# Performance work log

Hardware: AMD Instinct MI355X
Metric: run time of the kernel (lower is better)

The kernel has to match this reference:

```python
import jax, jax.numpy as jnp
import numpy as np

DIM = 512
FEAT = 64
BATCH = 2048

def setup_inputs() -> dict:
    key = jax.random.key(0)
    kx, kw, kb = jax.random.split(key, 3)
    x = jax.random.normal(kx, (BATCH, DIM, FEAT), dtype=jnp.float32)
    # torch Linear weight is [out, in]; emulate Kaiming-uniform-ish init scale
    bound = 1.0 / np.sqrt(FEAT)
    W = jax.random.uniform(kw, (DIM, FEAT, FEAT), dtype=jnp.float32, minval=-bound, maxval=bound)
    b = jax.random.uniform(kb, (DIM, FEAT), dtype=jnp.float32, minval=-bound, maxval=bound)
    return {"x": x, "W": W, "b": b}

def reference(x, W, b):
    # per-slice Linear: out[:, d, :] = x[:, d, :] @ W[d].T + b[d]
    # fused as one batched contraction over the feature (input) axis 'f'
    return jnp.einsum('bdf,dgf->bdg', x, W) + b[None, :, :]
```

## Files before the change

kernel.cpp:

```cpp
#include <hip/hip_runtime.h>
#include <hip/hip_bf16.h>

#define DIM  512
#define FEAT 64
#define BATCH 2048

#define DPB    64
#define NTILES 16

using bf16x8 = __attribute__((ext_vector_type(8))) short;
using f32x4  = __attribute__((ext_vector_type(4))) float;

typedef __attribute__((address_space(3))) float lds_f;
typedef __attribute__((address_space(1))) const float glb_f;

__device__ inline short f2bf(float f) {
    unsigned int u = __float_as_uint(f);
    u += 0x7fffu + ((u >> 16) & 1u);
    return (short)(u >> 16);
}

__device__ inline bf16x8 cvt8(float4 a, float4 b) {
    bf16x8 r;
    r[0] = f2bf(a.x); r[1] = f2bf(a.y); r[2] = f2bf(a.z); r[3] = f2bf(a.w);
    r[4] = f2bf(b.x); r[5] = f2bf(b.y); r[6] = f2bf(b.z); r[7] = f2bf(b.w);
    return r;
}

__global__ __launch_bounds__(256)
void w_prep(const float* __restrict__ W, short* __restrict__ ws) {
    const int d = blockIdx.x;
    const int t = threadIdx.x;
    const int l = t & 63, g0 = t >> 6;
#pragma unroll
    for (int h = 0; h < 2; ++h) {
        const int g8 = g0 + h * 4;
        const int mt = g8 & 3, ks = g8 >> 2;
        const float* src = W + ((size_t)d * FEAT + mt * 16 + (l & 15)) * FEAT
                             + ks * 32 + (l >> 4) * 8;
        *(bf16x8*)(ws + ((size_t)(d * 8 + g8) * 64 + l) * 8)
            = cvt8(*(const float4*)src, *(const float4*)(src + 4));
    }
}

template<bool PRE>
__global__ __launch_bounds__(256, 2)
void split_linear_main(const float* __restrict__ x,
                       const float* __restrict__ W,
                       const short* __restrict__ Wb,
                       const float* __restrict__ bias,
                       float* __restrict__ out)
{
    __shared__ float slot[2][16][256];

    const int id = blockIdx.x;
    const int dc = id & 7;
    const int rc = id >> 3;
    const int d0 = dc * DPB;
    const int b0 = rc * 16;

    const int tid  = threadIdx.x;
    const int wave = tid >> 6;
    const int lane = tid & 63;
    const int lr   = lane & 15;
    const int lk   = lane >> 4;

    auto stage = [&](int s, int t) {
#pragma unroll
        for (int i = 0; i < 4; ++i) {
            const int r = wave * 4 + i;
            const float* gp = x + ((size_t)(b0 + r) * DIM + d0 + t * 4) * FEAT
                                + (lane >> 4) * 64 + (((lane & 15) ^ (r & 7)) << 2);
            __builtin_amdgcn_global_load_lds((glb_f*)gp, (lds_f*)&slot[s][r][0], 16, 0, 0);
        }
    };

    const short* wbp = Wb + ((size_t)(d0 + wave)) * 4096 + lane * 8;
    const float* bsp = bias + (size_t)d0 * FEAT + lane * 4;

    auto LOADW = [&](bf16x8 (&wf)[8], f32x4& bv, int t) {
        if (PRE) {
            const short* wq = wbp + (size_t)t * 4 * 4096;
#pragma unroll
            for (int g = 0; g < 8; ++g)
                wf[g] = *(const bf16x8*)(wq + g * 512);
        } else {
            const float* wq = W + (size_t)(d0 + t * 4 + wave) * FEAT * FEAT;
#pragma unroll
            for (int g = 0; g < 8; ++g) {
                const int mt = g & 3, ks = g >> 2;
                const float* p = wq + (size_t)(mt * 16 + lr) * FEAT + ks * 32 + lk * 8;
                wf[g] = cvt8(*(const float4*)p, *(const float4*)(p + 4));
            }
        }
        bv = *(const f32x4*)(bsp + t * 256);
    };

    auto BODY = [&](bf16x8 (&wfc)[8], bf16x8 (&wfn)[8], f32x4& bvc, f32x4& bvn, int t) {
        const int s = t & 1;
        if (t == 0 || t == NTILES - 1)
            asm volatile("s_waitcnt vmcnt(4)" ::: "memory");
        else
            asm volatile("s_waitcnt vmcnt(8)" ::: "memory");
        __builtin_amdgcn_s_barrier();
        __builtin_amdgcn_sched_barrier(0);

        if (t + 1 < NTILES) LOADW(wfn, bvn, t + 1);

        const float* sl = &slot[s][0][0];
        const int rbase = lr * 256 + wave * 64;
        float4 p0a = *(const float4*)&sl[rbase + (((lk * 2 + 0) ^ (lr & 7)) << 2)];
        float4 p0b = *(const float4*)&sl[rbase + (((lk * 2 + 1) ^ (lr & 7)) << 2)];
        float4 p1a = *(const float4*)&sl[rbase + (((8 + lk * 2 + 0) ^ (lr & 7)) << 2)];
        float4 p1b = *(const float4*)&sl[rbase + (((8 + lk * 2 + 1) ^ (lr & 7)) << 2)];

        bf16x8 af0 = cvt8(p0a, p0b);
        bf16x8 af1 = cvt8(p1a, p1b);

        f32x4 acc[4] = {{0.f,0.f,0.f,0.f},{0.f,0.f,0.f,0.f},
                        {0.f,0.f,0.f,0.f},{0.f,0.f,0.f,0.f}};
#pragma unroll
        for (int mt = 0; mt < 4; ++mt)
            acc[mt] = __builtin_amdgcn_mfma_f32_16x16x32_bf16(wfc[mt],     af0, acc[mt], 0, 0, 0);
#pragma unroll
        for (int mt = 0; mt < 4; ++mt)
            acc[mt] = __builtin_amdgcn_mfma_f32_16x16x32_bf16(wfc[4 + mt], af1, acc[mt], 0, 0, 0);

        asm volatile("s_waitcnt lgkmcnt(0)" ::: "memory");
        __builtin_amdgcn_s_barrier();
        __builtin_amdgcn_sched_barrier(0);

        float* slw = &slot[s][0][0];
#pragma unroll
        for (int mt = 0; mt < 4; ++mt) {
            const int pc = (mt * 4 + lk) ^ (lr & 7);
            *(f32x4*)&slw[lr * 256 + wave * 64 + pc * 4] = acc[mt];
        }
        asm volatile("s_waitcnt lgkmcnt(0)" ::: "memory");
        __builtin_amdgcn_s_barrier();
        __builtin_amdgcn_sched_barrier(0);

#pragma unroll
        for (int j = 0; j < 4; ++j) {
            const int r = wave * 4 + j;
            f32x4 v = *(const f32x4*)&slw[r * 256 + (lane >> 4) * 64
                                          + (((lane & 15) ^ (r & 7)) << 2)];
            v += bvc;
            __builtin_nontemporal_store(v,
                (f32x4*)(out + ((size_t)(b0 + r) * DIM + d0 + t * 4) * FEAT + lane * 4));
        }
        __builtin_amdgcn_sched_barrier(0);
        if (t + 2 < NTILES) stage(s, t + 2);
        __builtin_amdgcn_sched_barrier(0);
    };

    bf16x8 wfA[8], wfB[8];
    f32x4 bvA, bvB;

    stage(0, 0);
    __builtin_amdgcn_sched_barrier(0);
    LOADW(wfA, bvA, 0);
    __builtin_amdgcn_sched_barrier(0);
    stage(1, 1);
    __builtin_amdgcn_sched_barrier(0);

#pragma unroll
    for (int t = 0; t < NTILES; t += 2) {
        BODY(wfA, wfB, bvA, bvB, t);
        BODY(wfB, wfA, bvB, bvA, t + 1);
    }
}

extern "C" void kernel_launch(void* const* d_in, const int* in_sizes, int n_in,
                              void* d_out, int out_size, void* d_ws, size_t ws_size,
                              hipStream_t stream) {
    const float* x    = (const float*)d_in[0];
    const float* W    = (const float*)d_in[1];
    const float* bias = (const float*)d_in[2];
    float* out        = (float*)d_out;

    const size_t WSNEED = (size_t)DIM * 8 * 64 * 8 * sizeof(short);
    dim3 block(256, 1, 1);
    dim3 grid((BATCH / 16) * (DIM / DPB), 1, 1);

    if (ws_size >= WSNEED) {
        short* ws = (short*)d_ws;
        w_prep<<<dim3(DIM), block, 0, stream>>>(W, ws);
        split_linear_main<true><<<grid, block, 0, stream>>>(x, nullptr, ws, bias, out);
    } else {
        split_linear_main<false><<<grid, block, 0, stream>>>(x, W, nullptr, bias, out);
    }
}
```

Before: 120.6 us.

## Give each wave private LDS slices and batch rows, dropping block barriers

Work is split so each block handles 16 d-slices and 64 batch rows, and each wave owns 16 batch rows with its own LDS staging buffers. All three s_barrier calls per tile are removed, since waves no longer share LDS. The weight and bias prefetch for the next tile now starts after the MFMAs rather than before the LDS reads. In exchange, all four waves load the same weight fragments, so weight traffic through L1 and L2 is four times larger. Waves also overwrite their staging buffer with async global-to-LDS loads without an explicit LDS wait.

Result: slower. 132.6 us (+9.9%).

```diff
diff --git a/kernel.cpp b/kernel.cpp
--- a/kernel.cpp
+++ b/kernel.cpp
@@ -5,7 +5,6 @@
 #define FEAT 64
 #define BATCH 2048
 
-#define DPB    64
 #define NTILES 16
 
 using bf16x8 = __attribute__((ext_vector_type(8))) short;
@@ -51,13 +50,13 @@
                        const float* __restrict__ bias,
                        float* __restrict__ out)
 {
-    __shared__ float slot[2][16][256];
+    __shared__ float slot[4][2][1024];
 
     const int id = blockIdx.x;
-    const int dc = id & 7;
-    const int rc = id >> 3;
-    const int d0 = dc * DPB;
-    const int b0 = rc * 16;
+    const int dc = id & 31;
+    const int rc = id >> 5;
+    const int d0 = dc * NTILES;
+    const int b0 = rc * 64;
 
     const int tid  = threadIdx.x;
     const int wave = tid >> 6;
@@ -65,27 +64,28 @@
     const int lr   = lane & 15;
     const int lk   = lane >> 4;
 
+    const int b0w  = b0 + wave * 16;
+
     auto stage = [&](int s, int t) {
 #pragma unroll
         for (int i = 0; i < 4; ++i) {
-            const int r = wave * 4 + i;
-            const float* gp = x + ((size_t)(b0 + r) * DIM + d0 + t * 4) * FEAT
-                                + (lane >> 4) * 64 + (((lane & 15) ^ (r & 7)) << 2);
-            __builtin_amdgcn_global_load_lds((glb_f*)gp, (lds_f*)&slot[s][r][0], 16, 0, 0);
+            const int r = i * 4 + (lane >> 4);
+            const int c = (lane & 15) ^ (r & 7);
+            const float* gp = x + ((size_t)(b0w + r) * DIM + d0 + t) * FEAT + c * 4;
+            __builtin_amdgcn_global_load_lds((glb_f*)gp,
+                                             (lds_f*)&slot[wave][s][i * 256],
+                                             16, 0, 0);
         }
     };
 
-    const short* wbp = Wb + ((size_t)(d0 + wave)) * 4096 + lane * 8;
-    const float* bsp = bias + (size_t)d0 * FEAT + lane * 4;
-
     auto LOADW = [&](bf16x8 (&wf)[8], f32x4& bv, int t) {
         if (PRE) {
-            const short* wq = wbp + (size_t)t * 4 * 4096;
+            const short* wq = Wb + (size_t)(d0 + t) * 4096 + lane * 8;
 #pragma unroll
             for (int g = 0; g < 8; ++g)
                 wf[g] = *(const bf16x8*)(wq + g * 512);
         } else {
-            const float* wq = W + (size_t)(d0 + t * 4 + wave) * FEAT * FEAT;
+            const float* wq = W + (size_t)(d0 + t) * FEAT * FEAT;
 #pragma unroll
             for (int g = 0; g < 8; ++g) {
                 const int mt = g & 3, ks = g >> 2;
@@ -93,8 +93,18 @@
                 wf[g] = cvt8(*(const float4*)p, *(const float4*)(p + 4));
             }
         }
-        bv = *(const f32x4*)(bsp + t * 256);
+        bv = *(const f32x4*)(bias + (size_t)(d0 + t) * FEAT + lr * 4);
     };
+
+    bf16x8 wfA[8], wfB[8];
+    f32x4 bvA, bvB;
+
+    stage(0, 0);
+    __builtin_amdgcn_sched_barrier(0);
+    LOADW(wfA, bvA, 0);
+    __builtin_amdgcn_sched_barrier(0);
+    stage(1, 1);
+    __builtin_amdgcn_sched_barrier(0);
 
     auto BODY = [&](bf16x8 (&wfc)[8], bf16x8 (&wfn)[8], f32x4& bvc, f32x4& bvn, int t) {
         const int s = t & 1;
@@ -102,17 +112,13 @@
             asm volatile("s_waitcnt vmcnt(4)" ::: "memory");
         else
             asm volatile("s_waitcnt vmcnt(8)" ::: "memory");
-        __builtin_amdgcn_s_barrier();
         __builtin_amdgcn_sched_barrier(0);
 
-        if (t + 1 < NTILES) LOADW(wfn, bvn, t + 1);
-
-        const float* sl = &slot[s][0][0];
-        const int rbase = lr * 256 + wave * 64;
-        float4 p0a = *(const float4*)&sl[rbase + (((lk * 2 + 0) ^ (lr & 7)) << 2)];
-        float4 p0b = *(const float4*)&sl[rbase + (((lk * 2 + 1) ^ (lr & 7)) << 2)];
-        float4 p1a = *(const float4*)&sl[rbase + (((8 + lk * 2 + 0) ^ (lr & 7)) << 2)];
-        float4 p1b = *(const float4*)&sl[rbase + (((8 + lk * 2 + 1) ^ (lr & 7)) << 2)];
+        float* sl = &slot[wave][s][0];
+        float4 p0a = *(const float4*)&sl[lr * 64 + (((lk * 2 + 0) ^ (lr & 7)) << 2)];
+        float4 p0b = *(const float4*)&sl[lr * 64 + (((lk * 2 + 1) ^ (lr & 7)) << 2)];
+        float4 p1a = *(const float4*)&sl[lr * 64 + (((8 + lk * 2 + 0) ^ (lr & 7)) << 2)];
+        float4 p1b = *(const float4*)&sl[lr * 64 + (((8 + lk * 2 + 1) ^ (lr & 7)) << 2)];
 
         bf16x8 af0 = cvt8(p0a, p0b);
         bf16x8 af1 = cvt8(p1a, p1b);
@@ -125,44 +131,34 @@
 #pragma unroll
         for (int mt = 0; mt < 4; ++mt)
             acc[mt] = __builtin_amdgcn_mfma_f32_16x16x32_bf16(wfc[4 + mt], af1, acc[mt], 0, 0, 0);
-
-        asm volatile("s_waitcnt lgkmcnt(0)" ::: "memory");
-        __builtin_amdgcn_s_barrier();
         __builtin_amdgcn_sched_barrier(0);
 
-        float* slw = &slot[s][0][0];
-#pragma unroll
-        for (int mt = 0; mt < 4; ++mt) {
-            const int pc = (mt * 4 + lk) ^ (lr & 7);
-            *(f32x4*)&slw[lr * 256 + wave * 64 + pc * 4] = acc[mt];
-        }
-        asm volatile("s_waitcnt lgkmcnt(0)" ::: "memory");
-        __builtin_amdgcn_s_barrier();
+        if (t + 1 < NTILES) LOADW(wfn, bvn, t + 1);
         __builtin_amdgcn_sched_barrier(0);
 
 #pragma unroll
+        for (int mt = 0; mt < 4; ++mt) {
+            const int c  = mt * 4 + lk;
+            const int pc = c ^ (lr & 7);
+            *(f32x4*)&sl[lr * 64 + pc * 4] = acc[mt];
+        }
+
+#pragma unroll
         for (int j = 0; j < 4; ++j) {
-            const int r = wave * 4 + j;
-            f32x4 v = *(const f32x4*)&slw[r * 256 + (lane >> 4) * 64
-                                          + (((lane & 15) ^ (r & 7)) << 2)];
+            const int rr  = j * 4 + (lane >> 4);
+            const int cc  = lane & 15;
+            const int pc2 = cc ^ (rr & 7);
+            f32x4 v = *(const f32x4*)&sl[rr * 64 + pc2 * 4];
             v += bvc;
             __builtin_nontemporal_store(v,
-                (f32x4*)(out + ((size_t)(b0 + r) * DIM + d0 + t * 4) * FEAT + lane * 4));
+                (f32x4*)(out + ((size_t)(b0w + rr) * DIM + d0 + t) * FEAT + cc * 4));
         }
         __builtin_amdgcn_sched_barrier(0);
-        if (t + 2 < NTILES) stage(s, t + 2);
+
+        if (t + 2 < NTILES)
+            stage(s, t + 2);
         __builtin_amdgcn_sched_barrier(0);
     };
-
-    bf16x8 wfA[8], wfB[8];
-    f32x4 bvA, bvB;
-
-    stage(0, 0);
-    __builtin_amdgcn_sched_barrier(0);
-    LOADW(wfA, bvA, 0);
-    __builtin_amdgcn_sched_barrier(0);
-    stage(1, 1);
-    __builtin_amdgcn_sched_barrier(0);
 
 #pragma unroll
     for (int t = 0; t < NTILES; t += 2) {
@@ -181,7 +177,7 @@
 
     const size_t WSNEED = (size_t)DIM * 8 * 64 * 8 * sizeof(short);
     dim3 block(256, 1, 1);
-    dim3 grid((BATCH / 16) * (DIM / DPB), 1, 1);
+    dim3 grid((DIM / NTILES) * (BATCH / 64), 1, 1);
 
     if (ws_size >= WSNEED) {
         short* ws = (short*)d_ws;
```
